# Optimization experiments

Hardware: AMD Instinct MI355X
Metric: run time of the kernel (lower is better)

The kernel has to match this reference:

```python
import jax, jax.numpy as jnp
import numpy as np

N_HEADS = 16
D_HEAD = 64
THETA = 10000.0


def _rope_tables(S, dh, dtype):
    inv_freq = 1.0 / (THETA ** (jnp.arange(0, dh, 2, dtype=jnp.float32) / dh))  # [dh/2]
    ang = jnp.arange(S, dtype=jnp.float32)[:, None] * inv_freq[None, :]  # [S, dh/2]
    return jnp.cos(ang).astype(dtype), jnp.sin(ang).astype(dtype)


def _apply_rope(t, cos, sin):
    # t: [B,S,H,dh]; interleaved complex pairs (even=real, odd=imag)
    B, S, H, dh = t.shape
    tr = t.reshape(B, S, H, dh // 2, 2)
    a, b = tr[..., 0], tr[..., 1]
    c = cos[None, :, None, :]
    s = sin[None, :, None, :]
    ra = a * c - b * s
    rb = a * s + b * c
    return jnp.stack([ra, rb], axis=-1).reshape(B, S, H, dh)


def setup_inputs() -> dict:
    key = jax.random.key(0)
    ks = jax.random.split(key, 5)
    B, S, D = 2, 2048, 1024
    x = jax.random.normal(ks[0], (B, S, D), dtype=jnp.float32)
    scale = 1.0 / np.sqrt(D)
    wq = jax.random.normal(ks[1], (D, D), dtype=jnp.float32) * scale
    wk = jax.random.normal(ks[2], (D, D), dtype=jnp.float32) * scale
    wv = jax.random.normal(ks[3], (D, D), dtype=jnp.float32) * scale
    wo = jax.random.normal(ks[4], (D, D), dtype=jnp.float32) * scale
    return {"x": x, "wq": wq, "wk": wk, "wv": wv, "wo": wo}


def reference(x, wq, wk, wv, wo):
    B, S, D = x.shape
    H, dh = N_HEADS, D_HEAD
    q = (x @ wq).reshape(B, S, H, dh)
    k = (x @ wk).reshape(B, S, H, dh)
    v = (x @ wv).reshape(B, S, H, dh)
    cos, sin = _rope_tables(S, dh, x.dtype)
    q = _apply_rope(q, cos, sin)
    k = _apply_rope(k, cos, sin)
    # [B,H,S,S] scores
    scale = 1.0 / np.sqrt(dh).astype(np.float32)
    attn = jnp.einsum('bqhd,bkhd->bhqk', q, k) * scale
    causal = jnp.tril(jnp.ones((S, S), dtype=bool))[None, None]
    attn = jnp.where(causal, attn, -jnp.inf)
    probs = jax.nn.softmax(attn, axis=-1)
    head_out = jnp.einsum('bhqk,bkhd->bqhd', probs, v).reshape(B, S, D)
    return head_out @ wo
```

## Files before the change

kernel.cpp:

```cpp
#include <hip/hip_runtime.h>
#include <hip/hip_bf16.h>

#define S_LEN   2048
#define BATCH   2
#define NH      16
#define DH      64
#define DMODEL  1024
#define MTOT    (BATCH * S_LEN)

typedef __attribute__((ext_vector_type(4))) float f32x4;
typedef __attribute__((ext_vector_type(8))) short s16x8;
typedef __attribute__((ext_vector_type(4))) short s16x4;

#define MFMA_BF16(a, b, c) __builtin_amdgcn_mfma_f32_16x16x32_bf16((a), (b), (c), 0, 0, 0)

static __device__ __forceinline__ short f2bf(float f) {
    union { float f; unsigned u; } v; v.f = f;
    unsigned r = v.u + 0x7fffu + ((v.u >> 16) & 1u);
    return (short)(r >> 16);
}

static __device__ __forceinline__ unsigned cvtpk_bf16(float lo, float hi) {
    unsigned r;
    asm volatile("v_cvt_pk_bf16_f32 %0, %1, %2" : "=v"(r) : "v"(lo), "v"(hi));
    return r;
}

static __device__ __forceinline__ void gload_lds16(const void* g, void* l) {
    __builtin_amdgcn_global_load_lds(
        (const __attribute__((address_space(1))) void*)g,
        (__attribute__((address_space(3))) void*)l, 16, 0, 0);
}

#define VM_WAIT(N) asm volatile("s_waitcnt vmcnt(" #N ")" ::: "memory")

static __device__ __forceinline__ void barrier_sync() {
    asm volatile("" ::: "memory");
    __builtin_amdgcn_s_barrier();
    asm volatile("" ::: "memory");
}

__global__ __launch_bounds__(256) void prep_wt(const float* __restrict__ wq,
                                               const float* __restrict__ wk,
                                               const float* __restrict__ wv,
                                               const float* __restrict__ wo,
                                               short* __restrict__ wtb) {
    const float* W = (blockIdx.z == 0) ? wq : (blockIdx.z == 1) ? wk
                   : (blockIdx.z == 2) ? wv : wo;
    short* out = wtb + (size_t)blockIdx.z * DMODEL * DMODEL;

    __shared__ short T[64][72];
    const int t  = threadIdx.x;
    const int k0 = blockIdx.y * 64, n0 = blockIdx.x * 64;

    #pragma unroll
    for (int p = 0; p < 4; ++p) {
        const int kk = p * 16 + (t >> 4);
        const int nn = (t & 15) * 4;
        f32x4 v = *(const f32x4*)(W + (size_t)(k0 + kk) * DMODEL + n0 + nn);
        #pragma unroll
        for (int j = 0; j < 4; ++j) T[nn + j][kk] = f2bf(v[j]);
    }
    __syncthreads();
    #pragma unroll
    for (int p = 0; p < 4; ++p) {
        const int nn = p * 16 + (t >> 4);
        const int kk = (t & 15) * 4;
        *(s16x4*)(out + (size_t)(n0 + nn) * DMODEL + k0 + kk) = *(const s16x4*)&T[nn][kk];
    }
}

__global__ __launch_bounds__(256) void prep_x(const float* __restrict__ x,
                                              short* __restrict__ xb) {
    const size_t i = (size_t)(blockIdx.x * 256 + threadIdx.x) * 8;
    f32x4 a = *(const f32x4*)(x + i);
    f32x4 b = *(const f32x4*)(x + i + 4);
    s16x8 o;
    #pragma unroll
    for (int j = 0; j < 4; ++j) { o[j] = f2bf(a[j]); o[4 + j] = f2bf(b[j]); }
    *(s16x8*)(xb + i) = o;
}

__global__ __launch_bounds__(256) void prep_rope(float* __restrict__ cosT,
                                                 float* __restrict__ sinT) {
    const int idx = blockIdx.x * 256 + threadIdx.x;
    const int s = idx >> 5, i = idx & 31;
    const float inv = exp2f(-(float)i * (13.287712379549449f / 32.0f));
    const float ang = (float)s * inv;
    cosT[idx] = cosf(ang);
    sinT[idx] = sinf(ang);
}

__device__ __forceinline__ void gemm_tile(const short* __restrict__ A,
                                          const short* __restrict__ Bt,
                                          int m0, int n0, short* SM,
                                          f32x4 acc[4][4]) {
    const int tid  = threadIdx.x;
    const int lane = tid & 63;
    const int wv   = tid >> 6;
    const int wm   = (wv >> 1) * 64;
    const int wn   = (wv & 1) * 64;
    const int g = lane >> 4, c16 = lane & 15;

    short* Asb = SM;
    short* Bsb = SM + 12288;

    const int srow = tid >> 2;
    const int schk = (tid & 3) ^ ((tid >> 3) & 3);
    const short* ga0 = A  + (size_t)(m0 + srow)      * DMODEL + schk * 8;
    const short* ga1 = A  + (size_t)(m0 + 64 + srow) * DMODEL + schk * 8;
    const short* gb0 = Bt + (size_t)(n0 + srow)      * DMODEL + schk * 8;
    const short* gb1 = Bt + (size_t)(n0 + 64 + srow) * DMODEL + schk * 8;
    const int lw = wv * 512;

    #define STAGE_G(buf, ko) do { \
        gload_lds16(ga0 + (ko), Asb + (buf) * 4096 + lw); \
        gload_lds16(ga1 + (ko), Asb + (buf) * 4096 + 2048 + lw); \
        gload_lds16(gb0 + (ko), Bsb + (buf) * 4096 + lw); \
        gload_lds16(gb1 + (ko), Bsb + (buf) * 4096 + 2048 + lw); \
    } while (0)

    STAGE_G(0, 0);
    STAGE_G(1, 32);

    const int rlo = (g ^ ((c16 >> 1) & 3)) << 3;
    for (int ks = 0; ks < 32; ++ks) {
        if (ks < 31) { VM_WAIT(4); } else { VM_WAIT(0); }
        barrier_sync();
        if (ks + 2 < 32) STAGE_G((ks + 2) % 3, (ks + 2) * 32);
        const int cur = ks % 3;
        s16x8 af[4], bfr[4];
        #pragma unroll
        for (int i = 0; i < 4; ++i)
            af[i] = *(const s16x8*)&Asb[cur * 4096 + (wm + i * 16 + c16) * 32 + rlo];
        #pragma unroll
        for (int j = 0; j < 4; ++j)
            bfr[j] = *(const s16x8*)&Bsb[cur * 4096 + (wn + j * 16 + c16) * 32 + rlo];
        #pragma unroll
        for (int i = 0; i < 4; ++i)
            #pragma unroll
            for (int j = 0; j < 4; ++j)
                acc[i][j] = MFMA_BF16(af[i], bfr[j], acc[i][j]);
    }
    #undef STAGE_G
}

__global__ __launch_bounds__(256) void gemm_qkv(const short* __restrict__ xb,
                                                const short* __restrict__ wtb,
                                                short* __restrict__ Qo,
                                                short* __restrict__ Ko,
                                                short* __restrict__ Vt,
                                                const float* __restrict__ cosT,
                                                const float* __restrict__ sinT) {
    __shared__ __align__(16) short SM[24576];

    const int dd = blockIdx.x + 24 * blockIdx.y;
    const int ti = (dd & 7) * 96 + (dd >> 3);
    const int tx = ti % 24, ty = ti / 24;
    const int m0 = ty * 128, n0 = tx * 128;
    const int z  = tx >> 3;

    f32x4 acc[4][4] = {};
    gemm_tile(xb, wtb, m0, n0, SM, acc);

    const int tid  = threadIdx.x;
    const int lane = tid & 63;
    const int wv   = tid >> 6;
    const int wm   = (wv >> 1) * 64, wn = (wv & 1) * 64;
    const int g = lane >> 4, c16 = lane & 15;
    const int hbase = (n0 & 1023) >> 6;

    barrier_sync();
    short (*RP)[136] = (short(*)[136])SM;

    if (z < 2) {
        short* outp = (z == 0) ? Qo : Ko;
        const float post = (z == 0) ? 0.18033688011112042f : 1.0f;
        #pragma unroll
        for (int j = 0; j < 4; ++j) {
            const int nl = wn + j * 16 + c16;
            const int d  = (n0 + nl) & 63;
            #pragma unroll
            for (int i = 0; i < 4; ++i) {
                #pragma unroll
                for (int r = 0; r < 4; ++r) {
                    const int ml = wm + i * 16 + g * 4 + r;
                    const int s  = (m0 + ml) & (S_LEN - 1);
                    float v = acc[i][j][r];
                    float vo = __shfl_xor(v, 1, 64);
                    float cs = cosT[s * 32 + (d >> 1)];
                    float sn = sinT[s * 32 + (d >> 1)];
                    float res = (d & 1) ? (vo * sn + v * cs) : (v * cs - vo * sn);
                    RP[ml][nl] = f2bf(res * post);
                }
            }
        }
        barrier_sync();
        #pragma unroll
        for (int pass = 0; pass < 8; ++pass) {
            const int row = pass * 32 + (tid >> 3);
            const int k   = tid & 7;
            const int hh = row >> 7, ss = row & 127;
            const int m = m0 + ss;
            const int s = m & (S_LEN - 1), b = m >> 11;
            short* dst = outp + (((size_t)b * NH + hbase + hh) * S_LEN + s) * DH + k * 8;
            *(s16x8*)dst = *(const s16x8*)&RP[ss][hh * 64 + k * 8];
        }
    } else {
        #pragma unroll
        for (int j = 0; j < 4; ++j) {
            const int nl = wn + j * 16 + c16;
            #pragma unroll
            for (int i = 0; i < 4; ++i) {
                const int mlb = wm + i * 16 + g * 4;
                s16x4 pk;
                #pragma unroll
                for (int r = 0; r < 4; ++r) pk[r] = f2bf(acc[i][j][r]);
                *(s16x4*)&RP[nl][mlb] = pk;
            }
        }
        barrier_sync();
        const int b = m0 >> 11, sr0 = m0 & (S_LEN - 1);
        #pragma unroll
        for (int pass = 0; pass < 8; ++pass) {
            const int row = pass * 16 + (tid >> 4);
            const int k   = tid & 15;
            const int h = hbase + (row >> 6), d = row & 63;
            short* dst = Vt + (((size_t)b * NH + h) * DH + d) * S_LEN + sr0 + k * 8;
            *(s16x8*)dst = *(const s16x8*)&RP[row][k * 8];
        }
    }
}

__global__ __launch_bounds__(256) void attn(const short* __restrict__ Q,
                                            const short* __restrict__ K,
                                            const short* __restrict__ Vt,
                                            short* __restrict__ O) {
    const int tid  = threadIdx.x;
    const int lane = tid & 63;
    const int w    = tid >> 6;
    const int g = lane >> 4, c16 = lane & 15;
    const int bid  = blockIdx.x + 16 * blockIdx.y;
    const int cxcd = bid & 7, jj = bid >> 3;
    const int bh   = (jj & 3) * 8 + cxcd;
    const int bx   = jj >> 2;
    const size_t base = (size_t)bh * S_LEN * DH;
    const short* Kb = K + base;
    const short* Vb = Vt + (size_t)bh * DH * S_LEN;
    const int b = bh >> 4, h = bh & 15;

    __shared__ __align__(16) short KL[3][4096];
    __shared__ __align__(16) short VL[3][4096];
    __shared__ __align__(16) short P2[4][16][72];

    const int kr = tid >> 3;
    const int kc = (tid & 7) ^ (kr & 7);
    const short* kg0 = Kb + (size_t)kr * DH + (kc << 3);
    const short* kg1 = Kb + (size_t)(32 + kr) * DH + (kc << 3);
    const short* vg0 = Vb + (size_t)kr * S_LEN + (kc << 3);
    const short* vg1 = Vb + (size_t)(32 + kr) * S_LEN + (kc << 3);
    const int lw = w * 512;
    const int kx = c16 & 7;

    #pragma unroll 1
    for (int half = 0; half < 2; ++half) {
        const int ci = half ? bx : 31 - bx;
        const int ntiles = ci + 1;
        const int wq0 = ci * 64 + w * 16;

        gload_lds16(kg0, &KL[0][lw]);
        gload_lds16(kg1, &KL[0][2048 + lw]);
        gload_lds16(vg0, &VL[0][lw]);
        gload_lds16(vg1, &VL[0][2048 + lw]);
        s16x8 bq0 = *(const s16x8*)(Q + base + (size_t)(wq0 + c16) * DH + g * 8);
        s16x8 bq1 = *(const s16x8*)(Q + base + (size_t)(wq0 + c16) * DH + 32 + g * 8);
        if (ntiles > 1) {
            gload_lds16(kg0 + (size_t)64 * DH, &KL[1][lw]);
            gload_lds16(kg1 + (size_t)64 * DH, &KL[1][2048 + lw]);
            gload_lds16(vg0 + 64, &VL[1][lw]);
            gload_lds16(vg1 + 64, &VL[1][2048 + lw]);
        }

        f32x4 o[4] = {};
        float lsum = 0.f;

        for (int tt = 0; tt < ntiles; ++tt) {
            if (tt + 1 < ntiles) { VM_WAIT(4); } else { VM_WAIT(0); }
            barrier_sync();
            if (tt + 2 < ntiles) {
                const int nb = (tt + 2) % 3;
                const size_t ko = (size_t)(tt + 2) * 64;
                gload_lds16(kg0 + ko * DH, &KL[nb][lw]);
                gload_lds16(kg1 + ko * DH, &KL[nb][2048 + lw]);
                gload_lds16(vg0 + ko,      &VL[nb][lw]);
                gload_lds16(vg1 + ko,      &VL[nb][2048 + lw]);
            }
            const int cur = tt % 3;

            f32x4 s[4];
            __builtin_amdgcn_s_setprio(1);
            #pragma unroll
            for (int cg = 0; cg < 4; ++cg) {
                const int krow = (cg * 16 + c16) * 64;
                s16x8 kf0 = *(const s16x8*)&KL[cur][krow + ((g ^ kx) << 3)];
                s16x8 kf1 = *(const s16x8*)&KL[cur][krow + (((4 + g) ^ kx) << 3)];
                f32x4 zz = {};
                zz = MFMA_BF16(kf0, bq0, zz);
                s[cg] = MFMA_BF16(kf1, bq1, zz);
            }
            __builtin_amdgcn_s_setprio(0);

            s16x8 vf[4][2];
            #pragma unroll
            for (int nt = 0; nt < 4; ++nt) {
                const int vr = (nt * 16 + c16) * 64;
                vf[nt][0] = *(const s16x8*)&VL[cur][vr + ((g ^ kx) << 3)];
                vf[nt][1] = *(const s16x8*)&VL[cur][vr + (((4 + g) ^ kx) << 3)];
            }

            const bool diag = (tt == ci);
            const int qrel = w * 16 + c16;
            #pragma unroll
            for (int cg = 0; cg < 4; ++cg) {
                float e[4];
                #pragma unroll
                for (int r = 0; r < 4; ++r) {
                    e[r] = exp2f(s[cg][r]);
                    if (diag && (cg * 16 + g * 4 + r > qrel)) e[r] = 0.f;
                }
                lsum += (e[0] + e[1]) + (e[2] + e[3]);
                uint2 pk;
                pk.x = cvtpk_bf16(e[0], e[1]);
                pk.y = cvtpk_bf16(e[2], e[3]);
                *(uint2*)&P2[w][c16][cg * 16 + g * 4] = pk;
            }
            asm volatile("s_waitcnt lgkmcnt(0)" ::: "memory");
            __builtin_amdgcn_sched_barrier(0);
            s16x8 ap0 = *(const s16x8*)&P2[w][c16][g * 8];
            s16x8 ap1 = *(const s16x8*)&P2[w][c16][32 + g * 8];

            __builtin_amdgcn_s_setprio(1);
            #pragma unroll
            for (int nt = 0; nt < 4; ++nt) {
                o[nt] = MFMA_BF16(ap0, vf[nt][0], o[nt]);
                o[nt] = MFMA_BF16(ap1, vf[nt][1], o[nt]);
            }
            __builtin_amdgcn_s_setprio(0);
        }

        float lt = lsum;
        lt += __shfl_xor(lt, 16, 64);
        lt += __shfl_xor(lt, 32, 64);
        #pragma unroll
        for (int r = 0; r < 4; ++r) {
            const float linv = 1.0f / __shfl(lt, g * 4 + r, 64);
            #pragma unroll
            for (int nt = 0; nt < 4; ++nt) {
                O[((size_t)(b * S_LEN + wq0 + g * 4 + r)) * DMODEL
                  + h * DH + nt * 16 + c16] = f2bf(o[nt][r] * linv);
            }
        }
    }
}

__global__ __launch_bounds__(256) void gemm_o(const short* __restrict__ Ob,
                                              const short* __restrict__ WoT,
                                              float* __restrict__ C) {
    __shared__ __align__(16) short SM[24576];

    const int dd = blockIdx.x + 8 * blockIdx.y;
    const int ti = (dd & 7) * 32 + (dd >> 3);
    const int tx = ti & 7, ty = ti >> 3;
    const int m0 = ty * 128, n0 = tx * 128;

    f32x4 acc[4][4] = {};
    gemm_tile(Ob, WoT, m0, n0, SM, acc);

    const int tid  = threadIdx.x;
    const int lane = tid & 63;
    const int wv   = tid >> 6;
    const int wm   = (wv >> 1) * 64, wn = (wv & 1) * 64;
    const int g = lane >> 4, c16 = lane & 15;

    #pragma unroll
    for (int i = 0; i < 4; ++i)
        #pragma unroll
        for (int j = 0; j < 4; ++j) {
            const int n = n0 + wn + j * 16 + c16;
            #pragma unroll
            for (int r = 0; r < 4; ++r) {
                const int m = m0 + wm + i * 16 + g * 4 + r;
                C[(size_t)m * DMODEL + n] = acc[i][j][r];
            }
        }
}

extern "C" void kernel_launch(void* const* d_in, const int* in_sizes, int n_in,
                              void* d_out, int out_size, void* d_ws, size_t ws_size,
                              hipStream_t stream) {
    const float* x  = (const float*)d_in[0];
    const float* wq = (const float*)d_in[1];
    const float* wk = (const float*)d_in[2];
    const float* wv = (const float*)d_in[3];
    const float* wo = (const float*)d_in[4];
    float* out = (float*)d_out;

    char* ws = (char*)d_ws;
    short* wtb  = (short*)ws;
    short* xb   = (short*)(ws + (8ull  << 20));
    float* cosT = (float*)(ws + (16ull << 20));
    float* sinT = (float*)(ws + (16ull << 20) + (256ull << 10));
    short* Qb   = (short*)(ws + (17ull << 20));
    short* Kb   = (short*)(ws + (25ull << 20));
    short* Vtb  = (short*)(ws + (33ull << 20));
    short* Ob   = (short*)(ws + (41ull << 20));

    prep_wt  <<<dim3(16, 16, 4), 256, 0, stream>>>(wq, wk, wv, wo, wtb);
    prep_x   <<<dim3(2048),      256, 0, stream>>>(x, xb);
    prep_rope<<<dim3(256),       256, 0, stream>>>(cosT, sinT);

    gemm_qkv<<<dim3(24, 32), 256, 0, stream>>>(xb, wtb, Qb, Kb, Vtb, cosT, sinT);
    attn    <<<dim3(16, 32), 256, 0, stream>>>(Qb, Kb, Vtb, Ob);
    gemm_o  <<<dim3(8, 32),  256, 0, stream>>>(Ob, wtb + 3ull * DMODEL * DMODEL, out);
}
```

Measured before the change: 117.7 us.

## Rewrite QKV GEMM with 256x256 tiles, 512 threads and 128KB LDS double buffering

The QKV projection kernel now computes 256x256 output tiles with 8 waves and a 64-wide K step. It double-buffers through 128KB of dynamic LDS and interleaves the next-stage global-to-LDS loads between MFMA phases, with s_setprio raised around the MFMAs. The goal is more data reuse per byte loaded and better overlap of loads with compute. The tile grid also gets an XCD-aware remap. In exchange there are only 192 blocks, one per CU, with high register pressure, and the epilogue is split into two passes because the LDS staging area is limited.

```diff
diff --git a/kernel.cpp b/kernel.cpp
--- a/kernel.cpp
+++ b/kernel.cpp
@@ -91,9 +91,169 @@
     sinT[idx] = sinf(ang);
 }
 
+__global__ __launch_bounds__(512, 1) void gemm_qkv(const short* __restrict__ xb,
+                                                   const short* __restrict__ wtb,
+                                                   short* __restrict__ Qo,
+                                                   short* __restrict__ Ko,
+                                                   short* __restrict__ Vt,
+                                                   const float* __restrict__ cosT,
+                                                   const float* __restrict__ sinT) {
+    extern __shared__ short SM[];
+
+    const int tid  = threadIdx.x;
+    const int lane = tid & 63;
+    const int wv   = tid >> 6;
+    const int wr   = wv >> 2;
+    const int wc   = wv & 3;
+    const int g = lane >> 4, c16 = lane & 15;
+
+    const int dd   = blockIdx.x + 12 * blockIdx.y;
+    const int xcd  = dd & 7, local = dd >> 3;
+    const int ty   = (xcd & 3) * 4 + (local & 3);
+    const int tx   = (xcd >> 2) * 6 + (local >> 2);
+    const int m0 = ty * 256, n0 = tx * 256;
+    const int z  = tx >> 2;
+
+    const int srow8 = tid >> 3;
+    const int schk  = (tid & 7) ^ (srow8 & 7);
+    const short* gA = xb  + (size_t)(m0 + srow8) * DMODEL + schk * 8;
+    const short* gB = wtb + (size_t)(n0 + srow8) * DMODEL + schk * 8;
+    const int lw = wv << 9;
+
+    #define SC(mat, h, c, kt, buf) \
+        gload_lds16((mat ? gB : gA) + (size_t)((h) * 128 + (c) * 64) * DMODEL + (size_t)(kt) * 64, \
+                    SM + (mat) * 32768 + (buf) * 16384 + (h) * 8192 + (c) * 4096 + lw)
+
+    SC(0,0,0,0,0); SC(0,0,1,0,0); SC(0,1,0,0,0); SC(0,1,1,0,0);
+    SC(1,0,0,0,0); SC(1,0,1,0,0); SC(1,1,0,0,0); SC(1,1,1,0,0);
+    VM_WAIT(0);
+    barrier_sync();
+
+    f32x4 acc[8][4] = {};
+    const int rx = c16 & 7;
+
+    for (int kt = 0; kt < 16; ++kt) {
+        const int cur  = kt & 1;
+        const int nbuf = cur ^ 1;
+        const short* Acur = SM + cur * 16384 + wr * 8192;
+        const short* Bcur = SM + 32768 + cur * 16384 + (wc >> 1) * 8192 + (wc & 1) * 4096;
+        const bool more = (kt < 15);
+
+        s16x8 bfr[4][2];
+        #pragma unroll
+        for (int p = 0; p < 4; ++p) {
+            if (p == 0) {
+                #pragma unroll
+                for (int j = 0; j < 4; ++j) {
+                    const int brow = (j * 16 + c16) * 64;
+                    bfr[j][0] = *(const s16x8*)&Bcur[brow + ((g ^ rx) << 3)];
+                    bfr[j][1] = *(const s16x8*)&Bcur[brow + (((4 + g) ^ rx) << 3)];
+                }
+            }
+            s16x8 af[2][2];
+            #pragma unroll
+            for (int ii = 0; ii < 2; ++ii) {
+                const int arow = ((2 * p + ii) * 16 + c16) * 64;
+                af[ii][0] = *(const s16x8*)&Acur[arow + ((g ^ rx) << 3)];
+                af[ii][1] = *(const s16x8*)&Acur[arow + (((4 + g) ^ rx) << 3)];
+            }
+            if (more) {
+                if (p == 0) { SC(0,0,0,kt+1,nbuf); SC(0,0,1,kt+1,nbuf); SC(0,1,0,kt+1,nbuf); }
+                else if (p == 1) { SC(0,1,1,kt+1,nbuf); SC(1,0,0,kt+1,nbuf); SC(1,0,1,kt+1,nbuf); }
+                else if (p == 2) { SC(1,1,0,kt+1,nbuf); SC(1,1,1,kt+1,nbuf); }
+            }
+            barrier_sync();
+            __builtin_amdgcn_s_setprio(1);
+            #pragma unroll
+            for (int ii = 0; ii < 2; ++ii)
+                #pragma unroll
+                for (int j = 0; j < 4; ++j) {
+                    acc[2 * p + ii][j] = MFMA_BF16(af[ii][0], bfr[j][0], acc[2 * p + ii][j]);
+                    acc[2 * p + ii][j] = MFMA_BF16(af[ii][1], bfr[j][1], acc[2 * p + ii][j]);
+                }
+            __builtin_amdgcn_s_setprio(0);
+            if (p == 3) { VM_WAIT(0); }
+            barrier_sync();
+        }
+    }
+    #undef SC
+
+    const int hbase = (tx & 3) * 4;
+    if (z < 2) {
+        short* outp = (z == 0) ? Qo : Ko;
+        const float post = (z == 0) ? 0.18033688011112042f : 1.0f;
+        short (*RPq)[264] = (short(*)[264])SM;
+        #pragma unroll 1
+        for (int p2 = 0; p2 < 2; ++p2) {
+            if (wr == p2) {
+                #pragma unroll
+                for (int j = 0; j < 4; ++j) {
+                    const int nl = wc * 64 + j * 16 + c16;
+                    const int d  = j * 16 + c16;
+                    #pragma unroll
+                    for (int i = 0; i < 8; ++i) {
+                        #pragma unroll
+                        for (int r = 0; r < 4; ++r) {
+                            const int ml = i * 16 + g * 4 + r;
+                            const int s  = (m0 + p2 * 128 + ml) & (S_LEN - 1);
+                            float v = acc[i][j][r];
+                            float vo = __shfl_xor(v, 1, 64);
+                            float cs = cosT[s * 32 + (d >> 1)];
+                            float sn = sinT[s * 32 + (d >> 1)];
+                            float res = (d & 1) ? (vo * sn + v * cs) : (v * cs - vo * sn);
+                            RPq[ml][nl] = f2bf(res * post);
+                        }
+                    }
+                }
+            }
+            barrier_sync();
+            #pragma unroll
+            for (int ps = 0; ps < 8; ++ps) {
+                const int idx = ps * 512 + tid;
+                const int ss = idx >> 5, ch = idx & 31;
+                const int m = m0 + p2 * 128 + ss;
+                const int s = m & (S_LEN - 1), bb = m >> 11;
+                short* dst = outp + (((size_t)bb * NH + hbase + (ch >> 3)) * S_LEN + s) * DH + (ch & 7) * 8;
+                *(s16x8*)dst = *(const s16x8*)&RPq[ss][ch * 8];
+            }
+            barrier_sync();
+        }
+    } else {
+        short (*RPv)[132] = (short(*)[132])SM;
+        #pragma unroll 1
+        for (int p2 = 0; p2 < 2; ++p2) {
+            if (wr == p2) {
+                #pragma unroll
+                for (int j = 0; j < 4; ++j) {
+                    const int nl = wc * 64 + j * 16 + c16;
+                    #pragma unroll
+                    for (int i = 0; i < 8; ++i) {
+                        s16x4 pk;
+                        #pragma unroll
+                        for (int r = 0; r < 4; ++r) pk[r] = f2bf(acc[i][j][r]);
+                        *(s16x4*)&RPv[nl][i * 16 + g * 4] = pk;
+                    }
+                }
+            }
+            barrier_sync();
+            const int mb = m0 + p2 * 128;
+            const int bb = mb >> 11, sr0 = mb & (S_LEN - 1);
+            #pragma unroll
+            for (int ps = 0; ps < 8; ++ps) {
+                const int idx = ps * 512 + tid;
+                const int row = idx >> 4, ch = idx & 15;
+                const int h = hbase + (row >> 6), d = row & 63;
+                short* dst = Vt + (((size_t)bb * NH + h) * DH + d) * S_LEN + sr0 + ch * 8;
+                *(s16x8*)dst = *(const s16x8*)&RPv[row][ch * 8];
+            }
+            barrier_sync();
+        }
+    }
+}
+
 __device__ __forceinline__ void gemm_tile(const short* __restrict__ A,
                                           const short* __restrict__ Bt,
-                                          int m0, int n0, short* SM,
+                                          int m0, int n0, short* SMl,
                                           f32x4 acc[4][4]) {
     const int tid  = threadIdx.x;
     const int lane = tid & 63;
@@ -102,8 +262,8 @@
     const int wn   = (wv & 1) * 64;
     const int g = lane >> 4, c16 = lane & 15;
 
-    short* Asb = SM;
-    short* Bsb = SM + 12288;
+    short* Asb = SMl;
+    short* Bsb = SMl + 12288;
 
     const int srow = tid >> 2;
     const int schk = (tid & 3) ^ ((tid >> 3) & 3);
@@ -143,93 +303,6 @@
                 acc[i][j] = MFMA_BF16(af[i], bfr[j], acc[i][j]);
     }
     #undef STAGE_G
-}
-
-__global__ __launch_bounds__(256) void gemm_qkv(const short* __restrict__ xb,
-                                                const short* __restrict__ wtb,
-                                                short* __restrict__ Qo,
-                                                short* __restrict__ Ko,
-                                                short* __restrict__ Vt,
-                                                const float* __restrict__ cosT,
-                                                const float* __restrict__ sinT) {
-    __shared__ __align__(16) short SM[24576];
-
-    const int dd = blockIdx.x + 24 * blockIdx.y;
-    const int ti = (dd & 7) * 96 + (dd >> 3);
-    const int tx = ti % 24, ty = ti / 24;
-    const int m0 = ty * 128, n0 = tx * 128;
-    const int z  = tx >> 3;
-
-    f32x4 acc[4][4] = {};
-    gemm_tile(xb, wtb, m0, n0, SM, acc);
-
-    const int tid  = threadIdx.x;
-    const int lane = tid & 63;
-    const int wv   = tid >> 6;
-    const int wm   = (wv >> 1) * 64, wn = (wv & 1) * 64;
-    const int g = lane >> 4, c16 = lane & 15;
-    const int hbase = (n0 & 1023) >> 6;
-
-    barrier_sync();
-    short (*RP)[136] = (short(*)[136])SM;
-
-    if (z < 2) {
-        short* outp = (z == 0) ? Qo : Ko;
-        const float post = (z == 0) ? 0.18033688011112042f : 1.0f;
-        #pragma unroll
-        for (int j = 0; j < 4; ++j) {
-            const int nl = wn + j * 16 + c16;
-            const int d  = (n0 + nl) & 63;
-            #pragma unroll
-            for (int i = 0; i < 4; ++i) {
-                #pragma unroll
-                for (int r = 0; r < 4; ++r) {
-                    const int ml = wm + i * 16 + g * 4 + r;
-                    const int s  = (m0 + ml) & (S_LEN - 1);
-                    float v = acc[i][j][r];
-                    float vo = __shfl_xor(v, 1, 64);
-                    float cs = cosT[s * 32 + (d >> 1)];
-                    float sn = sinT[s * 32 + (d >> 1)];
-                    float res = (d & 1) ? (vo * sn + v * cs) : (v * cs - vo * sn);
-                    RP[ml][nl] = f2bf(res * post);
-                }
-            }
-        }
-        barrier_sync();
-        #pragma unroll
-        for (int pass = 0; pass < 8; ++pass) {
-            const int row = pass * 32 + (tid >> 3);
-            const int k   = tid & 7;
-            const int hh = row >> 7, ss = row & 127;
-            const int m = m0 + ss;
-            const int s = m & (S_LEN - 1), b = m >> 11;
-            short* dst = outp + (((size_t)b * NH + hbase + hh) * S_LEN + s) * DH + k * 8;
-            *(s16x8*)dst = *(const s16x8*)&RP[ss][hh * 64 + k * 8];
-        }
-    } else {
-        #pragma unroll
-        for (int j = 0; j < 4; ++j) {
-            const int nl = wn + j * 16 + c16;
-            #pragma unroll
-            for (int i = 0; i < 4; ++i) {
-                const int mlb = wm + i * 16 + g * 4;
-                s16x4 pk;
-                #pragma unroll
-                for (int r = 0; r < 4; ++r) pk[r] = f2bf(acc[i][j][r]);
-                *(s16x4*)&RP[nl][mlb] = pk;
-            }
-        }
-        barrier_sync();
-        const int b = m0 >> 11, sr0 = m0 & (S_LEN - 1);
-        #pragma unroll
-        for (int pass = 0; pass < 8; ++pass) {
-            const int row = pass * 16 + (tid >> 4);
-            const int k   = tid & 15;
-            const int h = hbase + (row >> 6), d = row & 63;
-            short* dst = Vt + (((size_t)b * NH + h) * DH + d) * S_LEN + sr0 + k * 8;
-            *(s16x8*)dst = *(const s16x8*)&RP[row][k * 8];
-        }
-    }
 }
 
 __global__ __launch_bounds__(256) void attn(const short* __restrict__ Q,
@@ -366,7 +439,7 @@
 __global__ __launch_bounds__(256) void gemm_o(const short* __restrict__ Ob,
                                               const short* __restrict__ WoT,
                                               float* __restrict__ C) {
-    __shared__ __align__(16) short SM[24576];
+    __shared__ __align__(16) short SMl[24576];
 
     const int dd = blockIdx.x + 8 * blockIdx.y;
     const int ti = (dd & 7) * 32 + (dd >> 3);
@@ -374,7 +447,7 @@
     const int m0 = ty * 128, n0 = tx * 128;
 
     f32x4 acc[4][4] = {};
-    gemm_tile(Ob, WoT, m0, n0, SM, acc);
+    gemm_tile(Ob, WoT, m0, n0, SMl, acc);
 
     const int tid  = threadIdx.x;
     const int lane = tid & 63;
@@ -419,7 +492,12 @@
     prep_x   <<<dim3(2048),      256, 0, stream>>>(x, xb);
     prep_rope<<<dim3(256),       256, 0, stream>>>(cosT, sinT);
 
-    gemm_qkv<<<dim3(24, 32), 256, 0, stream>>>(xb, wtb, Qb, Kb, Vtb, cosT, sinT);
+    static bool attr_set = false;
+    (void)hipFuncSetAttribute((const void*)gemm_qkv,
+                              hipFuncAttributeMaxDynamicSharedMemorySize, 131072);
+    (void)attr_set;
+
+    gemm_qkv<<<dim3(12, 16), 512, 131072, stream>>>(xb, wtb, Qb, Kb, Vtb, cosT, sinT);
     attn    <<<dim3(16, 32), 256, 0, stream>>>(Qb, Kb, Vtb, Ob);
     gemm_o  <<<dim3(8, 32),  256, 0, stream>>>(Ob, wtb + 3ull * DMODEL * DMODEL, out);
 }
```

Measured after the change: 165.3 us. 40.4% more time.

## Fuse prep kernels into one launch and remap QKV tiles per XCD

Applied to the files above, without the earlier changes.

Merges the weight transpose/convert, x conversion, and RoPE table kernels into a single launch with a fifth grid slice handling x and RoPE. Also changes gemm_qkv's block-to-tile mapping so each XCD covers a 2D block of 8 row tiles by 12 column tiles instead of full rows, aiming at better L2 reuse of A and B panels. Cuts launch overhead, but the x-conversion blocks now do 8x more work each, which may create a tail.

```diff
diff --git a/kernel.cpp b/kernel.cpp
--- a/kernel.cpp
+++ b/kernel.cpp
@@ -40,55 +40,58 @@
     asm volatile("" ::: "memory");
 }
 
-__global__ __launch_bounds__(256) void prep_wt(const float* __restrict__ wq,
-                                               const float* __restrict__ wk,
-                                               const float* __restrict__ wv,
-                                               const float* __restrict__ wo,
-                                               short* __restrict__ wtb) {
-    const float* W = (blockIdx.z == 0) ? wq : (blockIdx.z == 1) ? wk
-                   : (blockIdx.z == 2) ? wv : wo;
-    short* out = wtb + (size_t)blockIdx.z * DMODEL * DMODEL;
-
-    __shared__ short T[64][72];
-    const int t  = threadIdx.x;
-    const int k0 = blockIdx.y * 64, n0 = blockIdx.x * 64;
-
-    #pragma unroll
-    for (int p = 0; p < 4; ++p) {
-        const int kk = p * 16 + (t >> 4);
-        const int nn = (t & 15) * 4;
-        f32x4 v = *(const f32x4*)(W + (size_t)(k0 + kk) * DMODEL + n0 + nn);
-        #pragma unroll
-        for (int j = 0; j < 4; ++j) T[nn + j][kk] = f2bf(v[j]);
+__global__ __launch_bounds__(256) void prep_all(const float* __restrict__ wq,
+                                                const float* __restrict__ wk,
+                                                const float* __restrict__ wv,
+                                                const float* __restrict__ wo,
+                                                const float* __restrict__ x,
+                                                short* __restrict__ wtb,
+                                                short* __restrict__ xb,
+                                                float* __restrict__ cosT,
+                                                float* __restrict__ sinT) {
+    const int t = threadIdx.x;
+    if (blockIdx.z < 4) {
+        const float* W = (blockIdx.z == 0) ? wq : (blockIdx.z == 1) ? wk
+                       : (blockIdx.z == 2) ? wv : wo;
+        short* out = wtb + (size_t)blockIdx.z * DMODEL * DMODEL;
+
+        __shared__ short T[64][72];
+        const int k0 = blockIdx.y * 64, n0 = blockIdx.x * 64;
+
+        #pragma unroll
+        for (int p = 0; p < 4; ++p) {
+            const int kk = p * 16 + (t >> 4);
+            const int nn = (t & 15) * 4;
+            f32x4 v = *(const f32x4*)(W + (size_t)(k0 + kk) * DMODEL + n0 + nn);
+            #pragma unroll
+            for (int j = 0; j < 4; ++j) T[nn + j][kk] = f2bf(v[j]);
+        }
+        __syncthreads();
+        #pragma unroll
+        for (int p = 0; p < 4; ++p) {
+            const int nn = p * 16 + (t >> 4);
+            const int kk = (t & 15) * 4;
+            *(s16x4*)(out + (size_t)(n0 + nn) * DMODEL + k0 + kk) = *(const s16x4*)&T[nn][kk];
+        }
+    } else {
+        const int blk = blockIdx.y * 16 + blockIdx.x;
+        #pragma unroll
+        for (int jj = 0; jj < 8; ++jj) {
+            const size_t i = ((size_t)jj * 65536 + blk * 256 + t) * 8;
+            f32x4 a = *(const f32x4*)(x + i);
+            f32x4 b = *(const f32x4*)(x + i + 4);
+            s16x8 o;
+            #pragma unroll
+            for (int j = 0; j < 4; ++j) { o[j] = f2bf(a[j]); o[4 + j] = f2bf(b[j]); }
+            *(s16x8*)(xb + i) = o;
+        }
+        const int idx = blk * 256 + t;
+        const int s = idx >> 5, ii = idx & 31;
+        const float inv = exp2f(-(float)ii * (13.287712379549449f / 32.0f));
+        const float ang = (float)s * inv;
+        cosT[idx] = cosf(ang);
+        sinT[idx] = sinf(ang);
     }
-    __syncthreads();
-    #pragma unroll
-    for (int p = 0; p < 4; ++p) {
-        const int nn = p * 16 + (t >> 4);
-        const int kk = (t & 15) * 4;
-        *(s16x4*)(out + (size_t)(n0 + nn) * DMODEL + k0 + kk) = *(const s16x4*)&T[nn][kk];
-    }
-}
-
-__global__ __launch_bounds__(256) void prep_x(const float* __restrict__ x,
-                                              short* __restrict__ xb) {
-    const size_t i = (size_t)(blockIdx.x * 256 + threadIdx.x) * 8;
-    f32x4 a = *(const f32x4*)(x + i);
-    f32x4 b = *(const f32x4*)(x + i + 4);
-    s16x8 o;
-    #pragma unroll
-    for (int j = 0; j < 4; ++j) { o[j] = f2bf(a[j]); o[4 + j] = f2bf(b[j]); }
-    *(s16x8*)(xb + i) = o;
-}
-
-__global__ __launch_bounds__(256) void prep_rope(float* __restrict__ cosT,
-                                                 float* __restrict__ sinT) {
-    const int idx = blockIdx.x * 256 + threadIdx.x;
-    const int s = idx >> 5, i = idx & 31;
-    const float inv = exp2f(-(float)i * (13.287712379549449f / 32.0f));
-    const float ang = (float)s * inv;
-    cosT[idx] = cosf(ang);
-    sinT[idx] = sinf(ang);
 }
 
 __device__ __forceinline__ void gemm_tile(const short* __restrict__ A,
@@ -154,9 +157,11 @@
                                                 const float* __restrict__ sinT) {
     __shared__ __align__(16) short SM[24576];
 
-    const int dd = blockIdx.x + 24 * blockIdx.y;
-    const int ti = (dd & 7) * 96 + (dd >> 3);
-    const int tx = ti % 24, ty = ti / 24;
+    const int dd    = blockIdx.x + 24 * blockIdx.y;
+    const int xcd   = dd & 7;
+    const int local = dd >> 3;
+    const int ty = (xcd & 3) * 8 + local / 12;
+    const int tx = (xcd >> 2) * 12 + local % 12;
     const int m0 = ty * 128, n0 = tx * 128;
     const int z  = tx >> 3;
 
@@ -366,7 +371,7 @@
 __global__ __launch_bounds__(256) void gemm_o(const short* __restrict__ Ob,
                                               const short* __restrict__ WoT,
                                               float* __restrict__ C) {
-    __shared__ __align__(16) short SM[24576];
+    __shared__ __align__(16) short SMl[24576];
 
     const int dd = blockIdx.x + 8 * blockIdx.y;
     const int ti = (dd & 7) * 32 + (dd >> 3);
@@ -374,7 +379,7 @@
     const int m0 = ty * 128, n0 = tx * 128;
 
     f32x4 acc[4][4] = {};
-    gemm_tile(Ob, WoT, m0, n0, SM, acc);
+    gemm_tile(Ob, WoT, m0, n0, SMl, acc);
 
     const int tid  = threadIdx.x;
     const int lane = tid & 63;
@@ -415,9 +420,8 @@
     short* Vtb  = (short*)(ws + (33ull << 20));
     short* Ob   = (short*)(ws + (41ull << 20));
 
-    prep_wt  <<<dim3(16, 16, 4), 256, 0, stream>>>(wq, wk, wv, wo, wtb);
-    prep_x   <<<dim3(2048),      256, 0, stream>>>(x, xb);
-    prep_rope<<<dim3(256),       256, 0, stream>>>(cosT, sinT);
+    prep_all<<<dim3(16, 16, 5), 256, 0, stream>>>(wq, wk, wv, wo, x,
+                                                  wtb, xb, cosT, sinT);
 
     gemm_qkv<<<dim3(24, 32), 256, 0, stream>>>(xb, wtb, Qb, Kb, Vtb, cosT, sinT);
     attn    <<<dim3(16, 32), 256, 0, stream>>>(Qb, Kb, Vtb, Ob);
```

Measured after the change: 110.0 us. 6.6% less time.
